# Kernel tuning notes

Measured on AMD Instinct MI355X. Metric: run time of the kernel, lower is better.

Reference implementation:

```python
import jax, jax.numpy as jnp
import numpy as np

B, L, D, H, O = 128, 256, 512, 1024, 2


def setup_inputs() -> dict:
    key = jax.random.key(0)
    ks = jax.random.split(key, 8)
    s = 1.0 / np.sqrt(H)
    sx = 1.0 / np.sqrt(D)
    return {
        "x": jax.random.normal(ks[0], (B, L, D), dtype=jnp.float32),
        "slen": jax.random.randint(ks[1], (B,), 0, L - 1),
        "Wh": jax.random.uniform(ks[2], (H, H), jnp.float32, -s, s),
        "bh": jax.random.uniform(ks[3], (H,), jnp.float32, -s, s),
        "Wx": jax.random.uniform(ks[4], (D, H), jnp.float32, -sx, sx),
        "bx": jax.random.uniform(ks[5], (H,), jnp.float32, -sx, sx),
        "Wo": jax.random.uniform(ks[6], (H, O), jnp.float32, -s, s),
        "bo": jax.random.uniform(ks[7], (O,), jnp.float32, -s, s),
    }


def reference(x, slen, Wh, bh, Wx, bx, Wo, bo):
    # x: (B, L, D) -> time-major (L, B, D)
    xT = jnp.transpose(x, (1, 0, 2))
    # input projection is time-independent: precompute Wx(x)+bx
    xp = xT @ Wx + bx  # (L, B, H)

    def step(carry, xpi):
        h, c = carry
        # All four 'gates' in the source share the same Wh/Wx, so a single
        # pre-activation z drives everything: i = f = o = sigmoid(z), g = tanh(z)
        z = h @ Wh + bh + xpi
        sg = jax.nn.sigmoid(z)
        g = jnp.tanh(z)
        c = sg * c + sg * g
        h = sg * jnp.tanh(c)
        return (h, c), h

    h0 = jnp.zeros((x.shape[0], Wh.shape[0]), dtype=x.dtype)
    _, hs = jax.lax.scan(step, (h0, h0), xp)  # (L, B, H)

    out = jax.nn.sigmoid(hs @ Wo + bo)  # (L, B, O)
    out = jnp.transpose(out, (1, 0, 2))  # (B, L, O)
    # positions il in [slen[b]+1, L) are overwritten with [0, 1]
    il = jnp.arange(out.shape[1])
    keep = (il[None, :] <= slen[:, None])[:, :, None]  # (B, L, 1)
    pad = jnp.array([0.0, 1.0], dtype=out.dtype)
    out = jnp.where(keep, out, pad)
    return out.reshape(-1, out.shape[-1])  # (B*L, O)
```

## Files before the change

### kernel.cpp

```cpp
#include <hip/hip_runtime.h>


#define B_ 128
#define L_ 256
#define D_ 512
#define H_ 1024

typedef __attribute__((ext_vector_type(8))) short short8;
typedef __attribute__((ext_vector_type(4))) float f32x4;
typedef __attribute__((ext_vector_type(2))) float f32x2;
typedef __attribute__((ext_vector_type(4))) unsigned short u16x4;
typedef __attribute__((ext_vector_type(4))) int i32x4;

__device__ __forceinline__ unsigned short f2bf(float f) {
    unsigned int u = __float_as_uint(f);
    return (unsigned short)((u + 0x8000u) >> 16);
}
__device__ __forceinline__ float bf2f(unsigned short s) {
    return __uint_as_float(((unsigned int)s) << 16);
}

__device__ __forceinline__ void st8(unsigned short* p, unsigned long long v) {
    __hip_atomic_store((unsigned long long*)p, v,
                       __ATOMIC_RELAXED, __HIP_MEMORY_SCOPE_AGENT);
}

template<int OFF>
__device__ __forceinline__ i32x4 ld16cc(const unsigned short* p) {
    i32x4 r;
    asm volatile("global_load_dwordx4 %0, %1, off offset:%2 sc0 sc1"
                 : "=v"(r) : "v"(p), "i"(OFF) : "memory");
    return r;
}
__device__ __forceinline__ void wait_vm4(i32x4& a, i32x4& b, i32x4& c, i32x4& d) {
    asm volatile("s_waitcnt vmcnt(4)" : "+v"(a), "+v"(b), "+v"(c), "+v"(d) :: "memory");
}
__device__ __forceinline__ void wait_vm0(i32x4& a, i32x4& b, i32x4& c, i32x4& d) {
    asm volatile("s_waitcnt vmcnt(0)" : "+v"(a), "+v"(b), "+v"(c), "+v"(d) :: "memory");
}
__device__ __forceinline__ void release_vm0() {
    asm volatile("s_waitcnt vmcnt(0)" ::: "memory");
}

__global__ __launch_bounds__(256) void k0_prep(
    const float* __restrict__ Wh, const float* __restrict__ Wx,
    const float* __restrict__ bh, const float* __restrict__ bx,
    unsigned short* __restrict__ Whb_t, unsigned short* __restrict__ Wxb_t,
    float* __restrict__ bxh, int* __restrict__ bar)
{
    __shared__ float tile[64][65];
    const int blk = blockIdx.x;
    const int t   = threadIdx.x;
    const int c   = t & 63, r0 = t >> 6;

    if (blk < 256) {
        const int tk = (blk >> 4) * 64, tn = (blk & 15) * 64;
#pragma unroll
        for (int i = 0; i < 16; ++i) {
            int r = i * 4 + r0;
            tile[r][c] = Wh[(size_t)(tk + r) * H_ + tn + c];
        }
        __syncthreads();
#pragma unroll
        for (int i = 0; i < 16; ++i) {
            int r = i * 4 + r0;
            Whb_t[(size_t)(tn + r) * H_ + tk + c] = f2bf(tile[c][r]);
        }
    } else if (blk < 384) {
        const int bi = blk - 256;
        const int tk = (bi >> 4) * 64, tn = (bi & 15) * 64;
#pragma unroll
        for (int i = 0; i < 16; ++i) {
            int r = i * 4 + r0;
            tile[r][c] = Wx[(size_t)(tk + r) * H_ + tn + c];
        }
        __syncthreads();
#pragma unroll
        for (int i = 0; i < 16; ++i) {
            int r = i * 4 + r0;
            Wxb_t[(size_t)(tn + r) * D_ + tk + c] = f2bf(tile[c][r]);
        }
    } else {
        for (int i = t; i < H_; i += 256) bxh[i] = bx[i] + bh[i];
        for (int i = t; i < 8 * 1024; i += 256) bar[i] = 0;
    }
}

__global__ __launch_bounds__(256) void k1_xproj(
    const float* __restrict__ x, const unsigned short* __restrict__ Wxb_t,
    const float* __restrict__ bxh, unsigned short* __restrict__ xp)
{
    const int nt   = blockIdx.x & 3;
    const int mt   = blockIdx.x >> 2;
    const int w    = threadIdx.x >> 6;
    const int lane = threadIdx.x & 63;
    const int m    = lane & 15, q = lane >> 4;
    const int m0   = mt * 64;
    const int l    = m0 >> 7;
    const int brow = (m0 & 127) + w * 16;
    const int n0   = nt * 256;

    const float* ap = x + ((size_t)(brow + m) * L_ + l) * D_ + q * 8;

    f32x4 acc[16];
#pragma unroll
    for (int t = 0; t < 16; ++t) acc[t] = (f32x4){0.f, 0.f, 0.f, 0.f};

#pragma unroll 4
    for (int kk = 0; kk < 16; ++kk) {
        f32x4 av0 = *(const f32x4*)(ap + kk * 32);
        f32x4 av1 = *(const f32x4*)(ap + kk * 32 + 4);
        short8 a8;
        a8[0] = (short)f2bf(av0[0]); a8[1] = (short)f2bf(av0[1]);
        a8[2] = (short)f2bf(av0[2]); a8[3] = (short)f2bf(av0[3]);
        a8[4] = (short)f2bf(av1[0]); a8[5] = (short)f2bf(av1[1]);
        a8[6] = (short)f2bf(av1[2]); a8[7] = (short)f2bf(av1[3]);
#pragma unroll
        for (int t = 0; t < 16; ++t) {
            short8 b8 = *(const short8*)(Wxb_t +
                        (size_t)(n0 + t * 16 + m) * D_ + kk * 32 + q * 8);
            acc[t] = __builtin_amdgcn_mfma_f32_16x16x32_bf16(b8, a8, acc[t], 0, 0, 0);
        }
    }

#pragma unroll
    for (int t = 0; t < 16; ++t) {
        const int c0 = n0 + t * 16 + q * 4;
        f32x4 bias = *(const f32x4*)(bxh + c0);
        u16x4 o;
#pragma unroll
        for (int r = 0; r < 4; ++r) o[r] = f2bf(acc[t][r] + bias[r]);
        *(u16x4*)(xp + ((size_t)l * B_ + brow + m) * H_ + c0) = o;
    }
}

__global__ __launch_bounds__(256, 1) void k2_scan(
    const unsigned short* __restrict__ Whb_t,
    const unsigned short* __restrict__ xp,
    unsigned short* __restrict__ hs,
    int* __restrict__ bar)
{
    __shared__ unsigned short buf[2][16][1032];

    const int g    = blockIdx.x & 7;
    const int wg   = blockIdx.x >> 3;
    const int tid  = threadIdx.x;
    const int w    = tid >> 6;
    const int lane = tid & 63;
    const int mb   = lane & 15, q = lane >> 4;
    const int b0   = g * 16;
    const int colw = wg * 64 + w * 16;

    short8 afrag[32];
    {
        const unsigned short* wp = Whb_t + (size_t)(colw + mb) * H_ + q * 8;
#pragma unroll
        for (int kk = 0; kk < 32; ++kk)
            asm volatile("global_load_dwordx4 %0, %1, off offset:%2"
                         : "=v"(afrag[kk]) : "v"(wp), "i"(kk * 64));
        asm volatile("s_waitcnt vmcnt(0)" ::: "memory");
#pragma unroll
        for (int kk = 0; kk < 32; ++kk)
            asm volatile("" : "+v"(afrag[kk]));
    }

    int* flags  = bar + g * 1024;
    int* myflag = flags + (wg * 4 + w) * 16;

    const int srow = tid >> 4;
    const int sci  = tid & 15;

    float c[4] = {0.f, 0.f, 0.f, 0.f};

    for (int l = 0; l < L_; ++l) {
        u16x4 xv = *(const u16x4*)(xp + ((size_t)l * B_ + b0 + mb) * H_ + colw + q * 4);

        unsigned short* lbuf = &buf[l & 1][0][0];
        if (l > 0) {
            while (true) {
                int f = __hip_atomic_load(flags + lane * 16,
                         __ATOMIC_RELAXED, __HIP_MEMORY_SCOPE_AGENT);
                if (__all(f >= l)) break;
            }
            const unsigned short* gp =
                hs + ((size_t)(l - 1) * B_ + b0 + srow) * H_ + sci * 8;
            i32x4 v0, v1, v2, v3, v4, v5, v6, v7;
            v0 = ld16cc<0>(gp);    v1 = ld16cc<256>(gp);
            v2 = ld16cc<512>(gp);  v3 = ld16cc<768>(gp);
            v4 = ld16cc<1024>(gp); v5 = ld16cc<1280>(gp);
            v6 = ld16cc<1536>(gp); v7 = ld16cc<1792>(gp);
            unsigned short* lp = lbuf + srow * 1032 + sci * 8;
            wait_vm4(v0, v1, v2, v3);
            *(i32x4*)(lp)        = v0;  *(i32x4*)(lp + 128)  = v1;
            *(i32x4*)(lp + 256)  = v2;  *(i32x4*)(lp + 384)  = v3;
            wait_vm0(v4, v5, v6, v7);
            *(i32x4*)(lp + 512)  = v4;  *(i32x4*)(lp + 640)  = v5;
            *(i32x4*)(lp + 768)  = v6;  *(i32x4*)(lp + 896)  = v7;
        }
        __syncthreads();

        f32x4 acc0 = {0.f,0.f,0.f,0.f}, acc1 = {0.f,0.f,0.f,0.f};
        f32x4 acc2 = {0.f,0.f,0.f,0.f}, acc3 = {0.f,0.f,0.f,0.f};
        if (l > 0) {
            const unsigned short* rp = lbuf + mb * 1032 + q * 8;
#pragma unroll
            for (int kb = 0; kb < 32; kb += 4) {
                short8 bb0 = *(const short8*)(rp + (kb + 0) * 32);
                short8 bb1 = *(const short8*)(rp + (kb + 1) * 32);
                short8 bb2 = *(const short8*)(rp + (kb + 2) * 32);
                short8 bb3 = *(const short8*)(rp + (kb + 3) * 32);
                acc0 = __builtin_amdgcn_mfma_f32_16x16x32_bf16(afrag[kb + 0], bb0, acc0, 0, 0, 0);
                acc1 = __builtin_amdgcn_mfma_f32_16x16x32_bf16(afrag[kb + 1], bb1, acc1, 0, 0, 0);
                acc2 = __builtin_amdgcn_mfma_f32_16x16x32_bf16(afrag[kb + 2], bb2, acc2, 0, 0, 0);
                acc3 = __builtin_amdgcn_mfma_f32_16x16x32_bf16(afrag[kb + 3], bb3, acc3, 0, 0, 0);
            }
        }
        u16x4 o;
#pragma unroll
        for (int r = 0; r < 4; ++r) {
            float z  = acc0[r] + acc1[r] + acc2[r] + acc3[r] + bf2f(xv[r]);
            float e  = __expf(-z);
            float sg = 1.f / (1.f + e);
            float gg = 2.f / (1.f + e * e) - 1.f;
            c[r] = sg * (c[r] + gg);
            float ec = __expf(-2.f * c[r]);
            float th = 2.f / (1.f + ec) - 1.f;
            o[r] = f2bf(sg * th);
        }
        union { u16x4 v; unsigned long long u; } hu;
        hu.v = o;
        st8(hs + ((size_t)l * B_ + b0 + mb) * H_ + colw + q * 4, hu.u);
        release_vm0();
        if (lane == 0)
            __hip_atomic_store(myflag, l + 1,
                               __ATOMIC_RELAXED, __HIP_MEMORY_SCOPE_AGENT);
    }
}

__global__ __launch_bounds__(256) void k3_out(
    const unsigned short* __restrict__ hs,
    const float* __restrict__ Wo, const float* __restrict__ bo,
    const int* __restrict__ slen, float* __restrict__ out)
{
    const int w    = threadIdx.x >> 6;
    const int lane = threadIdx.x & 63;
    const int r    = blockIdx.x * 4 + w;
    const int b    = r >> 8;
    const int l    = r & 255;

    const unsigned short* hp = hs + ((size_t)l * B_ + b) * H_ + lane * 16;
    const float* wp = Wo + (size_t)lane * 32;
    float u0 = 0.f, u1 = 0.f;
#pragma unroll
    for (int j0 = 0; j0 < 16; j0 += 8) {
        short8 hv = *(const short8*)(hp + j0);
#pragma unroll
        for (int j = 0; j < 8; ++j) {
            float h = bf2f((unsigned short)hv[j]);
            f32x2 wv = *(const f32x2*)(wp + (j0 + j) * 2);
            u0 += h * wv[0];
            u1 += h * wv[1];
        }
    }
#pragma unroll
    for (int off = 32; off; off >>= 1) {
        u0 += __shfl_down(u0, off);
        u1 += __shfl_down(u1, off);
    }
    if (lane == 0) {
        float o0, o1;
        if (l <= slen[b]) {
            o0 = 1.f / (1.f + __expf(-(u0 + bo[0])));
            o1 = 1.f / (1.f + __expf(-(u1 + bo[1])));
        } else {
            o0 = 0.f; o1 = 1.f;
        }
        out[(size_t)r * 2]     = o0;
        out[(size_t)r * 2 + 1] = o1;
    }
}

extern "C" void kernel_launch(void* const* d_in, const int* in_sizes, int n_in,
                              void* d_out, int out_size, void* d_ws, size_t ws_size,
                              hipStream_t stream)
{
    const float* x    = (const float*)d_in[0];
    const int*   slen = (const int*)d_in[1];
    const float* Wh   = (const float*)d_in[2];
    const float* bh   = (const float*)d_in[3];
    const float* Wx   = (const float*)d_in[4];
    const float* bx   = (const float*)d_in[5];
    const float* Wo   = (const float*)d_in[6];
    const float* bo   = (const float*)d_in[7];
    float* out = (float*)d_out;

    char* ws = (char*)d_ws;
    unsigned short* Whb_t = (unsigned short*)(ws);
    unsigned short* Wxb_t = (unsigned short*)(ws + (2u << 20));
    float*          bxh   = (float*)(ws + (3u << 20));
    int*            bar   = (int*)(ws + (3u << 20) + 65536);
    unsigned short* xp    = (unsigned short*)(ws + (4u << 20));
    unsigned short* hs    = (unsigned short*)(ws + (68u << 20));

    k0_prep<<<385, 256, 0, stream>>>(Wh, Wx, bh, bx, Whb_t, Wxb_t, bxh, bar);
    k1_xproj<<<2048, 256, 0, stream>>>(x, Wxb_t, bxh, xp);
    k2_scan<<<128, 256, 0, stream>>>(Whb_t, xp, hs, bar);
    k3_out<<<8192, 256, 0, stream>>>(hs, Wo, bo, slen, out);
}
```

Before: 1.362 ms.

## Rework scan-kernel barrier to per-workgroup flags with L2-scope polling and double-tile xproj

The recurrent scan kernel now publishes one flag per workgroup after a block-wide sync instead of one per wave. A single wave polls the 16 producer flags with loads that bypass only the near cache, and escalates to a system-coherent load every eighth round. The h-state reads drop the sc1 bit and the LDS row pitch is padded differently to change bank mapping. Separately, the input-projection kernel computes two 16-row batch tiles per wave so each Wx fragment load is reused twice, halving its grid. The relaxed coherence relies on all producer workgroups sharing the same L2 for correctness.

```diff
diff --git a/kernel.cpp b/kernel.cpp
--- a/kernel.cpp
+++ b/kernel.cpp
@@ -20,15 +20,31 @@
     return __uint_as_float(((unsigned int)s) << 16);
 }
 
-__device__ __forceinline__ void st8(unsigned short* p, unsigned long long v) {
+__device__ __forceinline__ void st8_ag(unsigned short* p, unsigned long long v) {
     __hip_atomic_store((unsigned long long*)p, v,
                        __ATOMIC_RELAXED, __HIP_MEMORY_SCOPE_AGENT);
 }
+__device__ __forceinline__ void st8_wg(unsigned short* p, unsigned long long v) {
+    *(volatile unsigned long long*)p = v;
+}
+
+__device__ __forceinline__ int ld_flag_l2(const int* p) {
+    int r;
+    asm volatile("global_load_dword %0, %1, off sc0\n\ts_waitcnt vmcnt(0)"
+                 : "=v"(r) : "v"(p) : "memory");
+    return r;
+}
+__device__ __forceinline__ int ld_flag_l3(const int* p) {
+    int r;
+    asm volatile("global_load_dword %0, %1, off sc0 sc1\n\ts_waitcnt vmcnt(0)"
+                 : "=v"(r) : "v"(p) : "memory");
+    return r;
+}
 
 template<int OFF>
-__device__ __forceinline__ i32x4 ld16cc(const unsigned short* p) {
+__device__ __forceinline__ i32x4 ld16_l2(const unsigned short* p) {
     i32x4 r;
-    asm volatile("global_load_dwordx4 %0, %1, off offset:%2 sc0 sc1"
+    asm volatile("global_load_dwordx4 %0, %1, off offset:%2 sc0"
                  : "=v"(r) : "v"(p), "i"(OFF) : "memory");
     return r;
 }
@@ -86,40 +102,46 @@
     }
 }
 
-__global__ __launch_bounds__(256) void k1_xproj(
+__global__ __launch_bounds__(256, 1) void k1_xproj(
     const float* __restrict__ x, const unsigned short* __restrict__ Wxb_t,
     const float* __restrict__ bxh, unsigned short* __restrict__ xp)
 {
     const int nt   = blockIdx.x & 3;
-    const int mt   = blockIdx.x >> 2;
+    const int l    = blockIdx.x >> 2;
     const int w    = threadIdx.x >> 6;
     const int lane = threadIdx.x & 63;
     const int m    = lane & 15, q = lane >> 4;
-    const int m0   = mt * 64;
-    const int l    = m0 >> 7;
-    const int brow = (m0 & 127) + w * 16;
     const int n0   = nt * 256;
-
-    const float* ap = x + ((size_t)(brow + m) * L_ + l) * D_ + q * 8;
-
-    f32x4 acc[16];
-#pragma unroll
-    for (int t = 0; t < 16; ++t) acc[t] = (f32x4){0.f, 0.f, 0.f, 0.f};
+    const int b0   = w * 32;
+
+    const float* ap0 = x + ((size_t)(b0 + m) * L_ + l) * D_ + q * 8;
+    const float* ap1 = ap0 + (size_t)16 * L_ * D_;
+
+    f32x4 acc0[16], acc1[16];
+#pragma unroll
+    for (int t = 0; t < 16; ++t) {
+        acc0[t] = (f32x4){0.f, 0.f, 0.f, 0.f};
+        acc1[t] = (f32x4){0.f, 0.f, 0.f, 0.f};
+    }
 
 #pragma unroll 4
     for (int kk = 0; kk < 16; ++kk) {
-        f32x4 av0 = *(const f32x4*)(ap + kk * 32);
-        f32x4 av1 = *(const f32x4*)(ap + kk * 32 + 4);
-        short8 a8;
-        a8[0] = (short)f2bf(av0[0]); a8[1] = (short)f2bf(av0[1]);
-        a8[2] = (short)f2bf(av0[2]); a8[3] = (short)f2bf(av0[3]);
-        a8[4] = (short)f2bf(av1[0]); a8[5] = (short)f2bf(av1[1]);
-        a8[6] = (short)f2bf(av1[2]); a8[7] = (short)f2bf(av1[3]);
+        f32x4 a0lo = *(const f32x4*)(ap0 + kk * 32);
+        f32x4 a0hi = *(const f32x4*)(ap0 + kk * 32 + 4);
+        f32x4 a1lo = *(const f32x4*)(ap1 + kk * 32);
+        f32x4 a1hi = *(const f32x4*)(ap1 + kk * 32 + 4);
+        short8 a80, a81;
+#pragma unroll
+        for (int j = 0; j < 4; ++j) {
+            a80[j]     = (short)f2bf(a0lo[j]); a80[j + 4] = (short)f2bf(a0hi[j]);
+            a81[j]     = (short)f2bf(a1lo[j]); a81[j + 4] = (short)f2bf(a1hi[j]);
+        }
 #pragma unroll
         for (int t = 0; t < 16; ++t) {
             short8 b8 = *(const short8*)(Wxb_t +
                         (size_t)(n0 + t * 16 + m) * D_ + kk * 32 + q * 8);
-            acc[t] = __builtin_amdgcn_mfma_f32_16x16x32_bf16(b8, a8, acc[t], 0, 0, 0);
+            acc0[t] = __builtin_amdgcn_mfma_f32_16x16x32_bf16(b8, a80, acc0[t], 0, 0, 0);
+            acc1[t] = __builtin_amdgcn_mfma_f32_16x16x32_bf16(b8, a81, acc1[t], 0, 0, 0);
         }
     }
 
@@ -127,10 +149,14 @@
     for (int t = 0; t < 16; ++t) {
         const int c0 = n0 + t * 16 + q * 4;
         f32x4 bias = *(const f32x4*)(bxh + c0);
-        u16x4 o;
-#pragma unroll
-        for (int r = 0; r < 4; ++r) o[r] = f2bf(acc[t][r] + bias[r]);
-        *(u16x4*)(xp + ((size_t)l * B_ + brow + m) * H_ + c0) = o;
+        u16x4 o0, o1;
+#pragma unroll
+        for (int r = 0; r < 4; ++r) {
+            o0[r] = f2bf(acc0[t][r] + bias[r]);
+            o1[r] = f2bf(acc1[t][r] + bias[r]);
+        }
+        *(u16x4*)(xp + ((size_t)l * B_ + b0 + m) * H_ + c0)      = o0;
+        *(u16x4*)(xp + ((size_t)l * B_ + b0 + 16 + m) * H_ + c0) = o1;
     }
 }
 
@@ -140,7 +166,7 @@
     unsigned short* __restrict__ hs,
     int* __restrict__ bar)
 {
-    __shared__ unsigned short buf[2][16][1032];
+    __shared__ unsigned short buf[2][16][1034];
 
     const int g    = blockIdx.x & 7;
     const int wg   = blockIdx.x >> 3;
@@ -165,7 +191,7 @@
     }
 
     int* flags  = bar + g * 1024;
-    int* myflag = flags + (wg * 4 + w) * 16;
+    int* myflag = flags + wg * 32;
 
     const int srow = tid >> 4;
     const int sci  = tid & 15;
@@ -177,19 +203,25 @@
 
         unsigned short* lbuf = &buf[l & 1][0][0];
         if (l > 0) {
-            while (true) {
-                int f = __hip_atomic_load(flags + lane * 16,
-                         __ATOMIC_RELAXED, __HIP_MEMORY_SCOPE_AGENT);
-                if (__all(f >= l)) break;
+            if (w == 0) {
+                const int* fp = flags + lane * 32;
+                int round = 0;
+                for (;;) {
+                    int f = l;
+                    if (lane < 16)
+                        f = ((++round & 7) == 0) ? ld_flag_l3(fp) : ld_flag_l2(fp);
+                    if (__all(f >= l)) break;
+                }
             }
+            __syncthreads();
             const unsigned short* gp =
                 hs + ((size_t)(l - 1) * B_ + b0 + srow) * H_ + sci * 8;
             i32x4 v0, v1, v2, v3, v4, v5, v6, v7;
-            v0 = ld16cc<0>(gp);    v1 = ld16cc<256>(gp);
-            v2 = ld16cc<512>(gp);  v3 = ld16cc<768>(gp);
-            v4 = ld16cc<1024>(gp); v5 = ld16cc<1280>(gp);
-            v6 = ld16cc<1536>(gp); v7 = ld16cc<1792>(gp);
-            unsigned short* lp = lbuf + srow * 1032 + sci * 8;
+            v0 = ld16_l2<0>(gp);    v1 = ld16_l2<256>(gp);
+            v2 = ld16_l2<512>(gp);  v3 = ld16_l2<768>(gp);
+            v4 = ld16_l2<1024>(gp); v5 = ld16_l2<1280>(gp);
+            v6 = ld16_l2<1536>(gp); v7 = ld16_l2<1792>(gp);
+            unsigned short* lp = lbuf + srow * 1034 + sci * 8;
             wait_vm4(v0, v1, v2, v3);
             *(i32x4*)(lp)        = v0;  *(i32x4*)(lp + 128)  = v1;
             *(i32x4*)(lp + 256)  = v2;  *(i32x4*)(lp + 384)  = v3;
@@ -202,7 +234,7 @@
         f32x4 acc0 = {0.f,0.f,0.f,0.f}, acc1 = {0.f,0.f,0.f,0.f};
         f32x4 acc2 = {0.f,0.f,0.f,0.f}, acc3 = {0.f,0.f,0.f,0.f};
         if (l > 0) {
-            const unsigned short* rp = lbuf + mb * 1032 + q * 8;
+            const unsigned short* rp = lbuf + mb * 1034 + q * 8;
 #pragma unroll
             for (int kb = 0; kb < 32; kb += 4) {
                 short8 bb0 = *(const short8*)(rp + (kb + 0) * 32);
@@ -229,11 +261,16 @@
         }
         union { u16x4 v; unsigned long long u; } hu;
         hu.v = o;
-        st8(hs + ((size_t)l * B_ + b0 + mb) * H_ + colw + q * 4, hu.u);
+        unsigned short* hp = hs + ((size_t)l * B_ + b0 + mb) * H_ + colw + q * 4;
+        st8_wg(hp, hu.u);
+        st8_ag(hp, hu.u);
         release_vm0();
-        if (lane == 0)
+        __syncthreads();
+        if (tid == 0) {
+            *(volatile int*)myflag = l + 1;
             __hip_atomic_store(myflag, l + 1,
                                __ATOMIC_RELAXED, __HIP_MEMORY_SCOPE_AGENT);
+        }
     }
 }
 
@@ -303,7 +340,7 @@
     unsigned short* hs    = (unsigned short*)(ws + (68u << 20));
 
     k0_prep<<<385, 256, 0, stream>>>(Wh, Wx, bh, bx, Whb_t, Wxb_t, bxh, bar);
-    k1_xproj<<<2048, 256, 0, stream>>>(x, Wxb_t, bxh, xp);
+    k1_xproj<<<1024, 256, 0, stream>>>(x, Wxb_t, bxh, xp);
     k2_scan<<<128, 256, 0, stream>>>(Whb_t, xp, hs, bar);
     k3_out<<<8192, 256, 0, stream>>>(hs, Wo, bo, slen, out);
 }
```

After: 2.223 ms. +63.3%, slower.
